# Performance work log

Measured on AMD Instinct MI355X. Metric: run time of the kernel, lower is better.

## Reference

```python
import jax, jax.numpy as jnp
import numpy as np

B, S, D_IN, D_EMB, H = 2, 2048, 1024, 1024, 16
HD = D_EMB // H

def setup_inputs() -> dict:
    key = jax.random.key(0)
    k1, k2, k3 = jax.random.split(key, 3)
    # xavier-uniform style scales
    lim_qkv = float(np.sqrt(6.0 / (D_IN + 3 * D_EMB)))
    lim_o = float(np.sqrt(6.0 / (D_EMB + D_EMB)))
    return {
        "x": jax.random.normal(k1, (B, S, D_IN), dtype=jnp.float32),
        "W_qkv": jax.random.uniform(k2, (3 * D_EMB, D_IN), minval=-lim_qkv, maxval=lim_qkv, dtype=jnp.float32),
        "b_qkv": jnp.zeros((3 * D_EMB,), dtype=jnp.float32),
        "W_o": jax.random.uniform(k3, (D_EMB, D_EMB), minval=-lim_o, maxval=lim_o, dtype=jnp.float32),
        "b_o": jnp.zeros((D_EMB,), dtype=jnp.float32),
    }

def reference(x, W_qkv, b_qkv, W_o, b_o):
    b, s, _ = x.shape
    qkv = x @ W_qkv.T + b_qkv                     # [B,S,3E]
    qkv = qkv.reshape(b, s, H, 3 * HD).transpose(0, 2, 1, 3)  # [B,H,S,3*HD]
    q, k, v = jnp.split(qkv, 3, axis=-1)          # each [B,H,S,HD]
    scale = 1.0 / np.sqrt(HD)
    attn = jax.nn.softmax(jnp.einsum('bhqd,bhkd->bhqk', q, k) * scale, axis=-1)
    vals = jnp.einsum('bhqk,bhkd->bhqd', attn, v) # [B,H,S,HD]
    vals = vals.transpose(0, 2, 1, 3).reshape(b, s, D_EMB)
    return vals @ W_o.T + b_o
```

## Files before the change

kernel.cpp:

```cpp
#include <hip/hip_runtime.h>
#include <hip/hip_bf16.h>

typedef unsigned short u16;
typedef unsigned int u32;
typedef __bf16 bf16x8 __attribute__((ext_vector_type(8)));
typedef float f32x4 __attribute__((ext_vector_type(4)));
typedef u32 u32x4 __attribute__((ext_vector_type(4)));

#define MFMA16(a, b, c) __builtin_amdgcn_mfma_f32_16x16x32_bf16((a), (b), (c), 0, 0, 0)

static __device__ __forceinline__ u16 f2bf(float f) {
  __hip_bfloat16 h = __float2bfloat16(f);
  return __builtin_bit_cast(u16, h);
}

static __device__ __forceinline__ u32 pack2(float a, float b) {
  return (u32)f2bf(a) | ((u32)f2bf(b) << 16);
}

static __device__ __forceinline__ bf16x8 ldbf8(const void* p) {
  return *reinterpret_cast<const bf16x8*>(p);
}

static __device__ __forceinline__ void gload_lds16(const void* g, void* l) {
  __builtin_amdgcn_global_load_lds(
      (const __attribute__((address_space(1))) u32*)g,
      (__attribute__((address_space(3))) u32*)l, 16, 0, 0);
}

__global__ void cvt_bf16(const float* __restrict__ s, u16* __restrict__ d, int n8) {
  int i = blockIdx.x * 256 + threadIdx.x;
  if (i >= n8) return;
  const float4* p = reinterpret_cast<const float4*>(s) + (size_t)i * 2;
  float4 a = p[0], b = p[1];
  uint4 o;
  o.x = (u32)f2bf(a.x) | ((u32)f2bf(a.y) << 16);
  o.y = (u32)f2bf(a.z) | ((u32)f2bf(a.w) << 16);
  o.z = (u32)f2bf(b.x) | ((u32)f2bf(b.y) << 16);
  o.w = (u32)f2bf(b.z) | ((u32)f2bf(b.w) << 16);
  reinterpret_cast<uint4*>(d)[i] = o;
}

template <bool BF16OUT>
__global__ __launch_bounds__(256, 3) void gemm_bt(const u16* __restrict__ A,
                                                  const u16* __restrict__ Bm,
                                                  const float* __restrict__ bias,
                                                  void* __restrict__ Cp,
                                                  int M, int N, int K) {
  __shared__ __align__(16) char As[128 * 64 * 2];
  __shared__ __align__(16) char Bs[128 * 64 * 2];
  const int tid = threadIdx.x;
  const int lane = tid & 63;
  const int wid = tid >> 6;
  const int fr = lane & 15, fg = lane >> 4;
  const int gx = gridDim.x, nwg = gx * gridDim.y;
  const int id = blockIdx.y * gx + blockIdx.x;
  const int nid = (id & 7) * (nwg >> 3) + (id >> 3);
  const int bm = nid / gx, bn = nid % gx;
  const int wm = (wid >> 1) * 64, wn = (wid & 1) * 64;

  f32x4 acc[4][4];
#pragma unroll
  for (int i = 0; i < 4; ++i)
#pragma unroll
    for (int j = 0; j < 4; ++j) acc[i][j] = (f32x4){0.f, 0.f, 0.f, 0.f};

  const int nk = K >> 6;
  for (int kt = 0; kt < nk; ++kt) {
#pragma unroll
    for (int it = 0; it < 4; ++it) {
      int q = it * 256 + tid;
      int row = q >> 3;
      int c = (q & 7) ^ (row & 7);
      gload_lds16(A + (size_t)(bm * 128 + row) * K + kt * 64 + c * 8, As + q * 16);
      gload_lds16(Bm + (size_t)(bn * 128 + row) * K + kt * 64 + c * 8, Bs + q * 16);
    }
    __syncthreads();
#pragma unroll
    for (int mk = 0; mk < 2; ++mk) {
      bf16x8 af[4], bfr[4];
#pragma unroll
      for (int i = 0; i < 4; ++i) {
        int row = wm + i * 16 + fr;
        af[i] = ldbf8(As + ((row * 128 + mk * 64 + fg * 16) ^ ((row & 7) << 4)));
      }
#pragma unroll
      for (int j = 0; j < 4; ++j) {
        int row = wn + j * 16 + fr;
        bfr[j] = ldbf8(Bs + ((row * 128 + mk * 64 + fg * 16) ^ ((row & 7) << 4)));
      }
#pragma unroll
      for (int i = 0; i < 4; ++i)
#pragma unroll
        for (int j = 0; j < 4; ++j) acc[i][j] = MFMA16(af[i], bfr[j], acc[i][j]);
    }
    __syncthreads();
  }

#pragma unroll
  for (int j = 0; j < 4; ++j) {
    int col = bn * 128 + wn + j * 16 + fr;
    float bv = bias[col];
#pragma unroll
    for (int i = 0; i < 4; ++i) {
#pragma unroll
      for (int r = 0; r < 4; ++r) {
        int row = bm * 128 + wm + i * 16 + fg * 4 + r;
        float v = acc[i][j][r] + bv;
        if (BF16OUT)
          ((u16*)Cp)[(size_t)row * N + col] = f2bf(v);
        else
          ((float*)Cp)[(size_t)row * N + col] = v;
      }
    }
  }
}

__global__ __launch_bounds__(256, 2) void attn_fwd(const u16* __restrict__ qkv,
                                                   u16* __restrict__ aout) {
  const int qt = blockIdx.x;
  const int bh = blockIdx.y;
  const int b = bh >> 4, h = bh & 15;
  const int tid = threadIdx.x, lane = tid & 63, wid = tid >> 6;
  const int fr = lane & 15, fg = (lane >> 4) & 3;

  __shared__ __align__(16) char Ks[2][64 * 128];
  __shared__ __align__(16) char VTs[2][64 * 128];

  const int q0 = qt * 128 + wid * 32;
  const size_t bS = (size_t)b * 2048;
  const u16* kbase = qkv + bS * 3072 + h * 192 + 64;
  const u16* vbase = qkv + bS * 3072 + h * 192 + 128;

  const int krow0 = tid >> 3, krow1 = 32 + (tid >> 3);
  const int kcol = (tid & 7) * 8;
  int kw0 = (krow0 * 128 + (tid & 7) * 16) ^ ((krow0 & 7) << 4);
  int kw1 = (krow1 * 128 + (tid & 7) * 16) ^ ((krow1 & 7) << 4);
  asm volatile("" : "+v"(kw0), "+v"(kw1));
  const int vs2 = (tid >> 3) * 2;
  const int vdc = (tid & 7) * 8;
  const int vm_ = vs2 >> 5, vG = (vs2 >> 2) & 3;
  const int vu = ((vs2 >> 4) & 1) * 2 + ((vs2 >> 1) & 1);
  const int vl0 = vm_ * 32 + ((vG ^ vu) << 3) + vu * 2;
  int wof[8];
#pragma unroll
  for (int j = 0; j < 8; ++j) {
    int d = vdc + j;
    wof[j] = ((d * 128 + vl0 * 2) ^ ((((d & 7) ^ ((d >> 3) & 7))) << 4));
    asm volatile("" : "+v"(wof[j]));
  }
  int kro[2];
#pragma unroll
  for (int mk = 0; mk < 2; ++mk) {
    kro[mk] = ((fr * 128 + mk * 64 + fg * 16) ^ ((fr & 7) << 4));
    asm volatile("" : "+v"(kro[mk]));
  }
  int vadr[4][2];
#pragma unroll
  for (int tp = 0; tp < 4; ++tp)
#pragma unroll
    for (int mk = 0; mk < 2; ++mk) {
      int d = tp * 16 + fr;
      int swz = (((d & 7) ^ ((d >> 3) & 7)) << 4);
      vadr[tp][mk] = ((d * 128 + mk * 64 + fg * 16) ^ swz);
      asm volatile("" : "+v"(vadr[tp][mk]));
    }

  bf16x8 qf[2][2];
#pragma unroll
  for (int qs = 0; qs < 2; ++qs)
#pragma unroll
    for (int mk = 0; mk < 2; ++mk) {
      bf16x8 v =
          ldbf8(qkv + (bS + q0 + qs * 16 + fr) * 3072 + h * 192 + mk * 32 + fg * 8);
#pragma unroll
      for (int e = 0; e < 8; ++e) v[e] = (__bf16)((float)v[e] * 0.1803368801f);
      qf[qs][mk] = v;
    }

  const u32 one2 = 0x3F803F80u;
  const u32x4 onev = {one2, one2, one2, one2};
  const bf16x8 onesf = __builtin_bit_cast(bf16x8, onev);
  float zs = 0.f;
  asm volatile("" : "+v"(zs));
  const f32x4 zacc = {zs, zs, zs, zs};

  f32x4 oacc0[4], oacc1[4];
#pragma unroll
  for (int t = 0; t < 4; ++t) {
    oacc0[t] = (f32x4){0.f, 0.f, 0.f, 0.f};
    oacc1[t] = (f32x4){0.f, 0.f, 0.f, 0.f};
  }
  f32x4 lacc0 = (f32x4){0.f, 0.f, 0.f, 0.f};
  f32x4 lacc1 = (f32x4){0.f, 0.f, 0.f, 0.f};

#define LOADT(S0, K0, K1, V0, V1)                                                    \
  K0 = *reinterpret_cast<const uint4*>(kbase + (size_t)((S0) + krow0) * 3072 + kcol); \
  K1 = *reinterpret_cast<const uint4*>(kbase + (size_t)((S0) + krow1) * 3072 + kcol); \
  V0 = *reinterpret_cast<const uint4*>(vbase + (size_t)((S0) + vs2) * 3072 + vdc);    \
  V1 = *reinterpret_cast<const uint4*>(vbase + (size_t)((S0) + vs2 + 1) * 3072 + vdc);

#define STAGE(BUF, K0, K1, V0, V1)                       \
  {                                                      \
    *reinterpret_cast<uint4*>(Ks[BUF] + kw0) = K0;       \
    *reinterpret_cast<uint4*>(Ks[BUF] + kw1) = K1;       \
    const u16* e0 = reinterpret_cast<const u16*>(&V0);   \
    const u16* e1 = reinterpret_cast<const u16*>(&V1);   \
    _Pragma("unroll") for (int j = 0; j < 8; ++j) {      \
      u32 w = (u32)e0[j] | ((u32)e1[j] << 16);           \
      *reinterpret_cast<u32*>(VTs[BUF] + wof[j]) = w;    \
    }                                                    \
  }

#define BAR()                                          \
  {                                                    \
    __builtin_amdgcn_sched_barrier(0);                 \
    asm volatile("s_waitcnt lgkmcnt(0)" ::: "memory"); \
    __builtin_amdgcn_s_barrier();                      \
    __builtin_amdgcn_sched_barrier(0);                 \
  }

#define COMPUTE(BUF)                                                           \
  {                                                                            \
    f32x4 sc0[4], sc1[4];                                                      \
    __builtin_amdgcn_s_setprio(1);                                             \
    _Pragma("unroll") for (int t = 0; t < 4; ++t) {                            \
      bf16x8 kf0 = ldbf8(Ks[BUF] + kro[0] + t * 2048);                         \
      bf16x8 kf1 = ldbf8(Ks[BUF] + kro[1] + t * 2048);                         \
      sc0[t] = MFMA16(kf0, qf[0][0], zacc);                                    \
      sc0[t] = MFMA16(kf1, qf[0][1], sc0[t]);                                  \
      sc1[t] = MFMA16(kf0, qf[1][0], zacc);                                    \
      sc1[t] = MFMA16(kf1, qf[1][1], sc1[t]);                                  \
    }                                                                          \
    __builtin_amdgcn_s_setprio(0);                                             \
    u32 Wp0[2][4], Wp1[2][4];                                                  \
    _Pragma("unroll") for (int t = 0; t < 4; ++t) {                            \
      Wp0[0][t] = pack2(__builtin_amdgcn_exp2f(sc0[t][0]),                     \
                        __builtin_amdgcn_exp2f(sc0[t][1]));                    \
      Wp0[1][t] = pack2(__builtin_amdgcn_exp2f(sc0[t][2]),                     \
                        __builtin_amdgcn_exp2f(sc0[t][3]));                    \
      Wp1[0][t] = pack2(__builtin_amdgcn_exp2f(sc1[t][0]),                     \
                        __builtin_amdgcn_exp2f(sc1[t][1]));                    \
      Wp1[1][t] = pack2(__builtin_amdgcn_exp2f(sc1[t][2]),                     \
                        __builtin_amdgcn_exp2f(sc1[t][3]));                    \
    }                                                                          \
    _Pragma("unroll") for (int mk = 0; mk < 2; ++mk) {                         \
      u32x4 pk0, pk1;                                                          \
      pk0.x = Wp0[0][2 * mk];                                                  \
      pk0.y = (u32)__shfl_xor((int)Wp0[1][2 * mk], 16);                        \
      pk0.z = (u32)__shfl_xor((int)Wp0[0][2 * mk + 1], 32);                    \
      pk0.w = (u32)__shfl_xor((int)Wp0[1][2 * mk + 1], 48);                    \
      pk1.x = Wp1[0][2 * mk];                                                  \
      pk1.y = (u32)__shfl_xor((int)Wp1[1][2 * mk], 16);                        \
      pk1.z = (u32)__shfl_xor((int)Wp1[0][2 * mk + 1], 32);                    \
      pk1.w = (u32)__shfl_xor((int)Wp1[1][2 * mk + 1], 48);                    \
      bf16x8 pa0 = __builtin_bit_cast(bf16x8, pk0);                            \
      bf16x8 pa1 = __builtin_bit_cast(bf16x8, pk1);                            \
      __builtin_amdgcn_s_setprio(1);                                           \
      lacc0 = MFMA16(pa0, onesf, lacc0);                                       \
      lacc1 = MFMA16(pa1, onesf, lacc1);                                       \
      _Pragma("unroll") for (int tp = 0; tp < 4; ++tp) {                       \
        bf16x8 vf = ldbf8(VTs[BUF] + vadr[tp][mk]);                            \
        oacc0[tp] = MFMA16(pa0, vf, oacc0[tp]);                                \
        oacc1[tp] = MFMA16(pa1, vf, oacc1[tp]);                                \
      }                                                                        \
      __builtin_amdgcn_s_setprio(0);                                           \
    }                                                                          \
  }

  uint4 ka0, ka1, va0, va1;
  uint4 kb0, kb1, vb0, vb1;
  LOADT(0, ka0, ka1, va0, va1);
  for (int kv = 0; kv < 32; kv += 2) {
    LOADT((kv + 1) * 64, kb0, kb1, vb0, vb1);
    STAGE(0, ka0, ka1, va0, va1);
    BAR();
    COMPUTE(0);
    {
      int s0n = (kv + 2 < 32) ? (kv + 2) * 64 : 0;
      LOADT(s0n, ka0, ka1, va0, va1);
    }
    STAGE(1, kb0, kb1, vb0, vb1);
    BAR();
    COMPUTE(1);
  }
#undef LOADT
#undef STAGE
#undef BAR
#undef COMPUTE

  {
    float invb0[4], invb1[4];
#pragma unroll
    for (int r = 0; r < 4; ++r) {
      invb0[r] = 1.f / lacc0[r];
      invb1[r] = 1.f / lacc1[r];
    }
#pragma unroll
    for (int tp = 0; tp < 4; ++tp) {
#pragma unroll
      for (int r = 0; r < 4; ++r) {
        int row0 = q0 + fg * 4 + r;
        aout[(bS + row0) * 1024 + h * 64 + tp * 16 + fr] =
            f2bf(oacc0[tp][r] * invb0[r]);
        int row1 = q0 + 16 + fg * 4 + r;
        aout[(bS + row1) * 1024 + h * 64 + tp * 16 + fr] =
            f2bf(oacc1[tp][r] * invb1[r]);
      }
    }
  }
}

extern "C" void kernel_launch(void* const* d_in, const int* in_sizes, int n_in,
                              void* d_out, int out_size, void* d_ws, size_t ws_size,
                              hipStream_t stream) {
  const float* x = (const float*)d_in[0];
  const float* Wqkv = (const float*)d_in[1];
  const float* bqkv = (const float*)d_in[2];
  const float* Wo = (const float*)d_in[3];
  const float* bo = (const float*)d_in[4];
  float* out = (float*)d_out;
  char* ws = (char*)d_ws;

  u16* xb = (u16*)(ws);
  u16* wqb = (u16*)(ws + 8388608);
  u16* wob = (u16*)(ws + 14680064);
  u16* qkvb = (u16*)(ws + 16777216);
  u16* attb = (u16*)(ws + 41943040);

  cvt_bf16<<<2048, 256, 0, stream>>>(x, xb, 524288);
  cvt_bf16<<<1536, 256, 0, stream>>>(Wqkv, wqb, 393216);
  cvt_bf16<<<512, 256, 0, stream>>>(Wo, wob, 131072);

  gemm_bt<true><<<dim3(24, 32), 256, 0, stream>>>(xb, wqb, bqkv, qkvb, 4096, 3072, 1024);
  attn_fwd<<<dim3(16, 32), 256, 0, stream>>>(qkvb, attb);
  gemm_bt<false><<<dim3(8, 32), 256, 0, stream>>>(attb, wob, bo, out, 4096, 1024, 1024);
}
```

Measured before the change: 114.4 us.

## Fuse bf16 conversions, remap attention blocks per XCD, double KV tile size

The three fp32-to-bf16 conversion launches are merged into a single kernel that picks its source and destination by index range, removing two launches. The attention kernel remaps block ids so that the query tiles of each (batch, head) land on the same XCD, which should improve L2 reuse of K/V. It also processes 128 KV rows per pipeline stage instead of 64, halving the number of barriers. The cost is doubled LDS use (64KB per block) and more registers for prefetched tiles, which may reduce occupancy below the 2 blocks per CU set by the launch bounds.

```diff
diff --git a/kernel.cpp b/kernel.cpp
--- a/kernel.cpp
+++ b/kernel.cpp
@@ -28,17 +28,28 @@
       (__attribute__((address_space(3))) u32*)l, 16, 0, 0);
 }
 
-__global__ void cvt_bf16(const float* __restrict__ s, u16* __restrict__ d, int n8) {
+__global__ void cvt_all(const float* __restrict__ x, const float* __restrict__ wq,
+                        const float* __restrict__ wo, u16* __restrict__ xb,
+                        u16* __restrict__ wqb, u16* __restrict__ wob) {
   int i = blockIdx.x * 256 + threadIdx.x;
-  if (i >= n8) return;
-  const float4* p = reinterpret_cast<const float4*>(s) + (size_t)i * 2;
+  const float* s;
+  u16* d;
+  int j;
+  if (i < 524288) {
+    s = x; d = xb; j = i;
+  } else if (i < 917504) {
+    s = wq; d = wqb; j = i - 524288;
+  } else {
+    s = wo; d = wob; j = i - 917504;
+  }
+  const float4* p = reinterpret_cast<const float4*>(s) + (size_t)j * 2;
   float4 a = p[0], b = p[1];
   uint4 o;
   o.x = (u32)f2bf(a.x) | ((u32)f2bf(a.y) << 16);
   o.y = (u32)f2bf(a.z) | ((u32)f2bf(a.w) << 16);
   o.z = (u32)f2bf(b.x) | ((u32)f2bf(b.y) << 16);
   o.w = (u32)f2bf(b.z) | ((u32)f2bf(b.w) << 16);
-  reinterpret_cast<uint4*>(d)[i] = o;
+  reinterpret_cast<uint4*>(d)[j] = o;
 }
 
 template <bool BF16OUT>
@@ -118,14 +129,16 @@
 
 __global__ __launch_bounds__(256, 2) void attn_fwd(const u16* __restrict__ qkv,
                                                    u16* __restrict__ aout) {
-  const int qt = blockIdx.x;
-  const int bh = blockIdx.y;
+  const int id = blockIdx.y * gridDim.x + blockIdx.x;
+  const int xcd = id & 7, slot = id >> 3;
+  const int bh = xcd * 4 + (slot >> 4);
+  const int qt = slot & 15;
   const int b = bh >> 4, h = bh & 15;
   const int tid = threadIdx.x, lane = tid & 63, wid = tid >> 6;
   const int fr = lane & 15, fg = (lane >> 4) & 3;
 
-  __shared__ __align__(16) char Ks[2][64 * 128];
-  __shared__ __align__(16) char VTs[2][64 * 128];
+  __shared__ __align__(16) char Ks[2][2][64 * 128];
+  __shared__ __align__(16) char VTs[2][2][64 * 128];
 
   const int q0 = qt * 128 + wid * 32;
   const size_t bS = (size_t)b * 2048;
@@ -194,22 +207,34 @@
   f32x4 lacc0 = (f32x4){0.f, 0.f, 0.f, 0.f};
   f32x4 lacc1 = (f32x4){0.f, 0.f, 0.f, 0.f};
 
-#define LOADT(S0, K0, K1, V0, V1)                                                    \
-  K0 = *reinterpret_cast<const uint4*>(kbase + (size_t)((S0) + krow0) * 3072 + kcol); \
-  K1 = *reinterpret_cast<const uint4*>(kbase + (size_t)((S0) + krow1) * 3072 + kcol); \
-  V0 = *reinterpret_cast<const uint4*>(vbase + (size_t)((S0) + vs2) * 3072 + vdc);    \
-  V1 = *reinterpret_cast<const uint4*>(vbase + (size_t)((S0) + vs2 + 1) * 3072 + vdc);
-
-#define STAGE(BUF, K0, K1, V0, V1)                       \
-  {                                                      \
-    *reinterpret_cast<uint4*>(Ks[BUF] + kw0) = K0;       \
-    *reinterpret_cast<uint4*>(Ks[BUF] + kw1) = K1;       \
-    const u16* e0 = reinterpret_cast<const u16*>(&V0);   \
-    const u16* e1 = reinterpret_cast<const u16*>(&V1);   \
-    _Pragma("unroll") for (int j = 0; j < 8; ++j) {      \
-      u32 w = (u32)e0[j] | ((u32)e1[j] << 16);           \
-      *reinterpret_cast<u32*>(VTs[BUF] + wof[j]) = w;    \
-    }                                                    \
+#define LOADT(S0, K0, K1, K2, K3, V0, V1, V2, V3)                                         \
+  K0 = *reinterpret_cast<const uint4*>(kbase + (size_t)((S0) + krow0) * 3072 + kcol);      \
+  K1 = *reinterpret_cast<const uint4*>(kbase + (size_t)((S0) + krow1) * 3072 + kcol);      \
+  K2 = *reinterpret_cast<const uint4*>(kbase + (size_t)((S0) + 64 + krow0) * 3072 + kcol); \
+  K3 = *reinterpret_cast<const uint4*>(kbase + (size_t)((S0) + 64 + krow1) * 3072 + kcol); \
+  V0 = *reinterpret_cast<const uint4*>(vbase + (size_t)((S0) + vs2) * 3072 + vdc);         \
+  V1 = *reinterpret_cast<const uint4*>(vbase + (size_t)((S0) + vs2 + 1) * 3072 + vdc);     \
+  V2 = *reinterpret_cast<const uint4*>(vbase + (size_t)((S0) + 64 + vs2) * 3072 + vdc);    \
+  V3 = *reinterpret_cast<const uint4*>(vbase + (size_t)((S0) + 64 + vs2 + 1) * 3072 + vdc);
+
+#define STAGEV1(VTP, V0, V1)                           \
+  {                                                    \
+    const u16* e0 = reinterpret_cast<const u16*>(&V0); \
+    const u16* e1 = reinterpret_cast<const u16*>(&V1); \
+    _Pragma("unroll") for (int j = 0; j < 8; ++j) {    \
+      u32 w = (u32)e0[j] | ((u32)e1[j] << 16);         \
+      *reinterpret_cast<u32*>((VTP) + wof[j]) = w;     \
+    }                                                  \
+  }
+
+#define STAGE(BUF, K0, K1, K2, K3, V0, V1, V2, V3)        \
+  {                                                       \
+    *reinterpret_cast<uint4*>(Ks[BUF][0] + kw0) = K0;     \
+    *reinterpret_cast<uint4*>(Ks[BUF][0] + kw1) = K1;     \
+    *reinterpret_cast<uint4*>(Ks[BUF][1] + kw0) = K2;     \
+    *reinterpret_cast<uint4*>(Ks[BUF][1] + kw1) = K3;     \
+    STAGEV1(VTs[BUF][0], V0, V1);                         \
+    STAGEV1(VTs[BUF][1], V2, V3);                         \
   }
 
 #define BAR()                                          \
@@ -220,13 +245,13 @@
     __builtin_amdgcn_sched_barrier(0);                 \
   }
 
-#define COMPUTE(BUF)                                                           \
+#define COMPUTE1(KSP, VTP)                                                     \
   {                                                                            \
     f32x4 sc0[4], sc1[4];                                                      \
     __builtin_amdgcn_s_setprio(1);                                             \
     _Pragma("unroll") for (int t = 0; t < 4; ++t) {                            \
-      bf16x8 kf0 = ldbf8(Ks[BUF] + kro[0] + t * 2048);                         \
-      bf16x8 kf1 = ldbf8(Ks[BUF] + kro[1] + t * 2048);                         \
+      bf16x8 kf0 = ldbf8((KSP) + kro[0] + t * 2048);                           \
+      bf16x8 kf1 = ldbf8((KSP) + kro[1] + t * 2048);                           \
       sc0[t] = MFMA16(kf0, qf[0][0], zacc);                                    \
       sc0[t] = MFMA16(kf1, qf[0][1], sc0[t]);                                  \
       sc1[t] = MFMA16(kf0, qf[1][0], zacc);                                    \
@@ -260,7 +285,7 @@
       lacc0 = MFMA16(pa0, onesf, lacc0);                                       \
       lacc1 = MFMA16(pa1, onesf, lacc1);                                       \
       _Pragma("unroll") for (int tp = 0; tp < 4; ++tp) {                       \
-        bf16x8 vf = ldbf8(VTs[BUF] + vadr[tp][mk]);                            \
+        bf16x8 vf = ldbf8((VTP) + vadr[tp][mk]);                               \
         oacc0[tp] = MFMA16(pa0, vf, oacc0[tp]);                                \
         oacc1[tp] = MFMA16(pa1, vf, oacc1[tp]);                                \
       }                                                                        \
@@ -268,25 +293,33 @@
     }                                                                          \
   }
 
-  uint4 ka0, ka1, va0, va1;
-  uint4 kb0, kb1, vb0, vb1;
-  LOADT(0, ka0, ka1, va0, va1);
-  for (int kv = 0; kv < 32; kv += 2) {
-    LOADT((kv + 1) * 64, kb0, kb1, vb0, vb1);
-    STAGE(0, ka0, ka1, va0, va1);
+#define COMPUTE(BUF)                \
+  {                                 \
+    COMPUTE1(Ks[BUF][0], VTs[BUF][0]); \
+    COMPUTE1(Ks[BUF][1], VTs[BUF][1]); \
+  }
+
+  uint4 ka0, ka1, ka2, ka3, va0, va1, va2, va3;
+  uint4 kb0, kb1, kb2, kb3, vb0, vb1, vb2, vb3;
+  LOADT(0, ka0, ka1, ka2, ka3, va0, va1, va2, va3);
+  for (int kv = 0; kv < 16; kv += 2) {
+    LOADT((kv + 1) * 128, kb0, kb1, kb2, kb3, vb0, vb1, vb2, vb3);
+    STAGE(0, ka0, ka1, ka2, ka3, va0, va1, va2, va3);
     BAR();
     COMPUTE(0);
     {
-      int s0n = (kv + 2 < 32) ? (kv + 2) * 64 : 0;
-      LOADT(s0n, ka0, ka1, va0, va1);
-    }
-    STAGE(1, kb0, kb1, vb0, vb1);
+      int s0n = (kv + 2 < 16) ? (kv + 2) * 128 : 0;
+      LOADT(s0n, ka0, ka1, ka2, ka3, va0, va1, va2, va3);
+    }
+    STAGE(1, kb0, kb1, kb2, kb3, vb0, vb1, vb2, vb3);
     BAR();
     COMPUTE(1);
   }
 #undef LOADT
+#undef STAGEV1
 #undef STAGE
 #undef BAR
+#undef COMPUTE1
 #undef COMPUTE
 
   {
@@ -328,9 +361,7 @@
   u16* qkvb = (u16*)(ws + 16777216);
   u16* attb = (u16*)(ws + 41943040);
 
-  cvt_bf16<<<2048, 256, 0, stream>>>(x, xb, 524288);
-  cvt_bf16<<<1536, 256, 0, stream>>>(Wqkv, wqb, 393216);
-  cvt_bf16<<<512, 256, 0, stream>>>(Wo, wob, 131072);
+  cvt_all<<<4096, 256, 0, stream>>>(x, Wqkv, Wo, xb, wqb, wob);
 
   gemm_bt<true><<<dim3(24, 32), 256, 0, stream>>>(xb, wqb, bqkv, qkvb, 4096, 3072, 1024);
   attn_fwd<<<dim3(16, 32), 256, 0, stream>>>(qkvb, attb);
```

Result: faster. 108.5 us (-5.1%).
